# Optimization experiments

Measured on AMD Instinct MI355X. Metric: run time of the kernel, lower is better.

## Reference

```python
import jax, jax.numpy as jnp
import numpy as np

VOCAB, EMB, HID, T, B = 10000, 1500, 1500, 35, 64
FORGET_BIAS = 1.0

def setup_inputs() -> dict:
    key = jax.random.key(0)
    ks = jax.random.split(key, 8)
    s = 0.02
    return {
        'x': jax.random.randint(ks[0], (T, B), 0, VOCAB),
        'y': jax.random.randint(ks[1], (T, B), 0, VOCAB),
        'embedding': jax.random.normal(ks[2], (VOCAB, EMB), jnp.float32) * s,
        'W0': jax.random.normal(ks[3], (EMB + HID, 4 * HID), jnp.float32) * s,
        'b0': jnp.zeros((4 * HID,), jnp.float32),
        'W1': jax.random.normal(ks[4], (2 * HID, 4 * HID), jnp.float32) * s,
        'b1': jnp.zeros((4 * HID,), jnp.float32),
        'softmax_w': jax.random.normal(ks[5], (HID, VOCAB), jnp.float32) * 0.1,
        'softmax_b': jnp.zeros((VOCAB,), jnp.float32),
    }

def _lstm_step(c, h, x, W, b):
    # TF LSTMCell: z = [x, h] @ W + b; gate order i, j, f, o; forget_bias added to f
    z = jnp.concatenate([x, h], axis=-1) @ W + b
    i, j, f, o = jnp.split(z, 4, axis=-1)
    c_new = c * jax.nn.sigmoid(f + FORGET_BIAS) + jax.nn.sigmoid(i) * jnp.tanh(j)
    h_new = jnp.tanh(c_new) * jax.nn.sigmoid(o)
    return c_new, h_new

def reference(x, y, embedding, W0, b0, W1, b1, softmax_w, softmax_b):
    inputs = embedding[x]  # [T, B, EMB] (time_major)
    zeros = jnp.zeros((B, HID), inputs.dtype)
    init = (zeros, zeros, zeros, zeros)  # (c0, h0, c1, h1)

    def step(carry, xt):
        c0, h0, c1, h1 = carry
        c0, h0 = _lstm_step(c0, h0, xt, W0, b0)
        c1, h1 = _lstm_step(c1, h1, h0, W1, b1)
        return (c0, h0, c1, h1), h1

    _, outputs = jax.lax.scan(step, init, inputs)  # [T, B, HID]
    logits = outputs.reshape(-1, HID) @ softmax_w + softmax_b  # [T*B, VOCAB]
    logp = jax.nn.log_softmax(logits, axis=-1)
    tgt = y.reshape(-1)
    nll = -jnp.take_along_axis(logp, tgt[:, None], axis=-1)[:, 0]
    loss = jnp.sum(nll) / B  # sequence_loss_by_example with unit weights, / batch_size
    return loss
```

## Files before the change

kernel.cpp:

```cpp
#include <hip/hip_runtime.h>
#include <math.h>

#define TT 35
#define BB 64
#define EMB 1500
#define HID 1500
#define VOCAB 10000
#define KT 3072
#define KG 768
#define NCH 24
#define KH 1536
#define KGH 384
#define NCHH 12
#define KLP 1504
#define NBLK 158
#define MROWS 2240
#define MPAD 2304
#define LBLK 94
#define ZXN 6000
#define FORGET_BIAS 1.0f

typedef __bf16 bf16x8 __attribute__((ext_vector_type(8)));
typedef float f32x4 __attribute__((ext_vector_type(4)));

__device__ __forceinline__ unsigned short f2bf(float f) {
    unsigned int u = __builtin_bit_cast(unsigned int, f);
    u += 0x7fffu + ((u >> 16) & 1u);
    return (unsigned short)(u >> 16);
}
__device__ __forceinline__ float bf2f(unsigned short u) {
    unsigned int v = ((unsigned int)u) << 16;
    return __builtin_bit_cast(float, v);
}
__device__ __forceinline__ float sigmoidf_(float x) { return 1.0f / (1.0f + expf(-x)); }

#define GLOAD_LDS16(gp, lp) __builtin_amdgcn_global_load_lds( \
    (const __attribute__((address_space(1))) void*)(gp),      \
    (__attribute__((address_space(3))) void*)(lp), 16, 0, 0)

__global__ __launch_bounds__(256) void convT(const float* __restrict__ W,
                                             unsigned short* __restrict__ WT,
                                             int K, int N, int KP) {
    __shared__ float tile[32][33];
    int tx = threadIdx.x, ty = threadIdx.y;
    int n0 = blockIdx.x * 32, k0 = blockIdx.y * 32;
#pragma unroll
    for (int i = 0; i < 4; ++i) {
        int k = k0 + ty + 8 * i, n = n0 + tx;
        tile[ty + 8 * i][tx] = (k < K && n < N) ? W[(size_t)k * N + n] : 0.f;
    }
    __syncthreads();
#pragma unroll
    for (int i = 0; i < 4; ++i) {
        int n = n0 + ty + 8 * i, k = k0 + tx;
        if (n < N) WT[(size_t)n * KP + k] = f2bf(tile[tx][ty + 8 * i]);
    }
}

__global__ __launch_bounds__(256) void embed_kernel(const int* __restrict__ x,
                                                    const float* __restrict__ emb,
                                                    unsigned short* __restrict__ Ae) {
    int tok = blockIdx.x;
    int v = x[tok];
    const float* src = emb + (size_t)v * EMB;
    unsigned short* dst = Ae + (size_t)tok * KH;
    for (int i = threadIdx.x; i < EMB; i += 256) dst[i] = f2bf(src[i]);
}

__global__ __launch_bounds__(256) void zx_gemm(const unsigned short* __restrict__ A,
                                               const unsigned short* __restrict__ WT,
                                               unsigned short* __restrict__ Zx) {
    __shared__ __align__(16) unsigned char smem[32768];
    int orig = blockIdx.x;
    int xcd = orig & 7, j = orig >> 3;
    int mb, bn;
    if (xcd < 7) { bn = xcd * 6 + j % 6; mb = j / 6; }
    else { if (j >= 90) return; bn = 42 + j % 5; mb = j / 5; }
    int n0 = bn * 128;

    int tid = threadIdx.x;
    int wv = tid >> 6, lane = tid & 63;
    int wr = wv >> 1, wc = wv & 1;
    int quad = lane >> 4, l16 = lane & 15;
    int rr = lane >> 2;
    int ks = (lane & 3) ^ (rr & 3);
    const unsigned short* gA[2]; const unsigned short* gB[2];
    int ldsA[2], ldsB[2];
#pragma unroll
    for (int i = 0; i < 2; ++i) {
        int r16 = wv * 2 + i;
        int ra = mb * 128 + r16 * 16 + rr;
        gA[i] = A + (size_t)ra * KH + ks * 8;
        ldsA[i] = r16 * 1024;
        int rb = n0 + r16 * 16 + rr;
        if (rb > 5999) rb = 5999;
        gB[i] = WT + (size_t)rb * KH + ks * 8;
        ldsB[i] = 8192 + r16 * 1024;
    }
    int sw16 = (quad ^ (l16 & 3)) * 16;
    int aoff[4], boff[4];
#pragma unroll
    for (int f = 0; f < 4; ++f) {
        aoff[f] = (wr * 64 + f * 16 + l16) * 64 + sw16;
        boff[f] = 8192 + (wc * 64 + f * 16 + l16) * 64 + sw16;
    }
    f32x4 acc[4][4];
#pragma unroll
    for (int i = 0; i < 4; ++i)
#pragma unroll
        for (int jj = 0; jj < 4; ++jj) acc[i][jj] = (f32x4){0.f, 0.f, 0.f, 0.f};

#pragma unroll
    for (int i = 0; i < 2; ++i) {
        GLOAD_LDS16(gA[i], smem + ldsA[i]);
        GLOAD_LDS16(gB[i], smem + ldsB[i]);
    }
    __syncthreads();
    for (int c = 0; c < KH / 32; ++c) {
        int buf = c & 1;
        if (c + 1 < KH / 32) {
            int ob = (buf ^ 1) * 16384;
#pragma unroll
            for (int i = 0; i < 2; ++i) {
                GLOAD_LDS16(gA[i] + (c + 1) * 32, smem + ob + ldsA[i]);
                GLOAD_LDS16(gB[i] + (c + 1) * 32, smem + ob + ldsB[i]);
            }
        }
        const unsigned char* base = smem + buf * 16384;
        bf16x8 a[4], b[4];
#pragma unroll
        for (int f = 0; f < 4; ++f) {
            a[f] = *(const bf16x8*)(base + aoff[f]);
            b[f] = *(const bf16x8*)(base + boff[f]);
        }
#pragma unroll
        for (int ar = 0; ar < 4; ++ar)
#pragma unroll
            for (int cb = 0; cb < 4; ++cb)
                acc[ar][cb] = __builtin_amdgcn_mfma_f32_16x16x32_bf16(a[ar], b[cb], acc[ar][cb], 0, 0, 0);
        __syncthreads();
    }
#pragma unroll
    for (int ar = 0; ar < 4; ++ar)
#pragma unroll
        for (int cb = 0; cb < 4; ++cb)
#pragma unroll
            for (int r2 = 0; r2 < 4; ++r2) {
                int row = mb * 128 + wr * 64 + ar * 16 + quad * 4 + r2;
                int col = n0 + wc * 64 + cb * 16 + l16;
                if (col < ZXN) Zx[(size_t)row * ZXN + col] = f2bf(acc[ar][cb][r2]);
            }
}

__global__ __launch_bounds__(1024) void lstm_pair(
        const unsigned short* __restrict__ A_0, const unsigned short* __restrict__ WT_0,
        const float* __restrict__ bias_0, float* __restrict__ cst_0,
        unsigned short* __restrict__ d1_0, int s1_0, unsigned short* __restrict__ d2_0, int s2_0,
        const unsigned short* __restrict__ zx_0,
        const unsigned short* __restrict__ A_1, const unsigned short* __restrict__ WT_1,
        const float* __restrict__ bias_1, float* __restrict__ cst_1,
        unsigned short* __restrict__ d1_1, int s1_1, unsigned short* __restrict__ d2_1, int s2_1) {
    __shared__ __align__(16) unsigned char smem[131072];

    const unsigned short* A;  const unsigned short* WT;
    const float* bias;        float* cst;
    unsigned short* d1; int s1; unsigned short* d2; int s2;
    const unsigned short* zx;
    int nb, kstr, kgK, nch;
    if (blockIdx.x < LBLK) {
        if (!A_0) return;
        A = A_0; WT = WT_0; bias = bias_0; cst = cst_0;
        d1 = d1_0; s1 = s1_0; d2 = d2_0; s2 = s2_0;
        zx = zx_0; kstr = KH; kgK = KGH; nch = NCHH;
        nb = blockIdx.x;
    } else {
        if (!A_1) return;
        A = A_1; WT = WT_1; bias = bias_1; cst = cst_1;
        d1 = d1_1; s1 = s1_1; d2 = d2_1; s2 = s2_1;
        zx = nullptr; kstr = KT; kgK = KG; nch = NCH;
        nb = blockIdx.x - LBLK;
    }

    int tid = threadIdx.x;
    int wv = tid >> 6, lane = tid & 63;
    int mt = wv & 3, kg = wv >> 2;
    int quad = lane >> 4, l16 = lane & 15;
    int col = nb * 16 + l16;

    int rr = lane >> 2, p = lane & 3;
    int sp = p ^ (rr & 3);
    int kbase = kg * kgK;
    int q0 = mt * 2, q1 = q0 + 1;
    const unsigned short* gp[2];
    int ldsoff[2];
#pragma unroll
    for (int ii = 0; ii < 2; ++ii) {
        int q = ii ? q1 : q0;
        if (q < 4) {
            gp[ii] = A + (size_t)(16 * q + rr) * kstr + kbase + sp * 8;
        } else {
            int g = q - 4;
            int ci = nb * 16 + rr; if (ci > HID - 1) ci = HID - 1;
            gp[ii] = WT + (size_t)(g * HID + ci) * kstr + kbase + sp * 8;
        }
        ldsoff[ii] = ((q >> 2) * 4 + kg) * 4096 + (q & 3) * 1024;
    }

    int swz = (quad ^ (l16 & 3)) * 16;
    int aoff = (0 * 4 + kg) * 4096 + (mt * 16 + l16) * 64 + swz;
    int boff = (1 * 4 + kg) * 4096 + l16 * 64 + swz;

    f32x4 acc0 = {0.f,0.f,0.f,0.f}, acc1 = acc0, acc2 = acc0, acc3 = acc0;

#pragma unroll
    for (int ci = 0; ci < 3; ++ci) {
        GLOAD_LDS16(gp[0] + ci * 32, smem + ci * 32768 + ldsoff[0]);
        GLOAD_LDS16(gp[1] + ci * 32, smem + ci * 32768 + ldsoff[1]);
    }

    for (int c = 0; c < nch; ++c) {
        asm volatile("s_waitcnt vmcnt(4)" ::: "memory");
        __builtin_amdgcn_sched_barrier(0);
        __builtin_amdgcn_s_barrier();
        int cs = (c + 3 < nch) ? (c + 3) : (nch - 1);
        int bs_ = (c + 3) & 3;
        GLOAD_LDS16(gp[0] + cs * 32, smem + bs_ * 32768 + ldsoff[0]);
        GLOAD_LDS16(gp[1] + cs * 32, smem + bs_ * 32768 + ldsoff[1]);
        const unsigned char* base = smem + (c & 3) * 32768;
        bf16x8 a  = *(const bf16x8*)(base + aoff);
        bf16x8 b0 = *(const bf16x8*)(base + boff);
        bf16x8 b1 = *(const bf16x8*)(base + boff + 1024);
        bf16x8 b2 = *(const bf16x8*)(base + boff + 2048);
        bf16x8 b3 = *(const bf16x8*)(base + boff + 3072);
        __builtin_amdgcn_s_setprio(1);
        acc0 = __builtin_amdgcn_mfma_f32_16x16x32_bf16(a, b0, acc0, 0, 0, 0);
        acc1 = __builtin_amdgcn_mfma_f32_16x16x32_bf16(a, b1, acc1, 0, 0, 0);
        acc2 = __builtin_amdgcn_mfma_f32_16x16x32_bf16(a, b2, acc2, 0, 0, 0);
        acc3 = __builtin_amdgcn_mfma_f32_16x16x32_bf16(a, b3, acc3, 0, 0, 0);
        __builtin_amdgcn_s_setprio(0);
    }
    asm volatile("s_waitcnt vmcnt(0)" ::: "memory");
    __builtin_amdgcn_sched_barrier(0);
    __syncthreads();

    float* red = (float*)smem;
    if (kg > 0) {
        int w = (kg - 1) * 4 + mt;
#pragma unroll
        for (int r = 0; r < 4; ++r) {
            red[(w * 64 + lane) * 16 + r]      = acc0[r];
            red[(w * 64 + lane) * 16 + 4 + r]  = acc1[r];
            red[(w * 64 + lane) * 16 + 8 + r]  = acc2[r];
            red[(w * 64 + lane) * 16 + 12 + r] = acc3[r];
        }
    }
    __syncthreads();
    if (kg == 0) {
#pragma unroll
        for (int k2 = 0; k2 < 3; ++k2) {
            int w = k2 * 4 + mt;
#pragma unroll
            for (int r = 0; r < 4; ++r) {
                acc0[r] += red[(w * 64 + lane) * 16 + r];
                acc1[r] += red[(w * 64 + lane) * 16 + 4 + r];
                acc2[r] += red[(w * 64 + lane) * 16 + 8 + r];
                acc3[r] += red[(w * 64 + lane) * 16 + 12 + r];
            }
        }
        if (col < HID) {
            float bi = bias[col], bj = bias[HID + col];
            float bf_ = bias[2 * HID + col], bo = bias[3 * HID + col];
#pragma unroll
            for (int r = 0; r < 4; ++r) {
                int row = mt * 16 + quad * 4 + r;
                float zi = acc0[r] + bi;
                float zj = acc1[r] + bj;
                float zf = acc2[r] + bf_;
                float zo = acc3[r] + bo;
                if (zx) {
                    const unsigned short* zr = zx + (size_t)row * ZXN;
                    zi += bf2f(zr[col]);
                    zj += bf2f(zr[HID + col]);
                    zf += bf2f(zr[2 * HID + col]);
                    zo += bf2f(zr[3 * HID + col]);
                }
                int ci = row * HID + col;
                float cn = cst[ci] * sigmoidf_(zf + FORGET_BIAS) + sigmoidf_(zi) * tanhf(zj);
                float hn = tanhf(cn) * sigmoidf_(zo);
                cst[ci] = cn;
                unsigned short hb = f2bf(hn);
                d1[(size_t)row * s1 + col] = hb;
                if (d2) d2[(size_t)row * s2 + col] = hb;
            }
        }
    }
}

__global__ __launch_bounds__(256) void logits_fold(const unsigned short* __restrict__ A,
                                                   const unsigned short* __restrict__ WT,
                                                   const float* __restrict__ sb,
                                                   const int* __restrict__ y,
                                                   float2* __restrict__ partials,
                                                   float* __restrict__ tgtlog) {
    __shared__ __align__(16) unsigned char smem[32768];

    int orig = blockIdx.x;
    int xcd = orig & 7, j = orig >> 3;
    int mb, bn;
    if (xcd < 7) { bn = xcd * 10 + j % 10; mb = j / 10; }
    else { if (j >= 162) return; bn = 70 + j % 9; mb = j / 9; }
    int n0 = bn * 128;

    int tid = threadIdx.x;
    int wv = tid >> 6, lane = tid & 63;
    int wr = wv >> 1, wc = wv & 1;
    int quad = lane >> 4, l16 = lane & 15;

    int rr = lane >> 2;
    int ks = (lane & 3) ^ (rr & 3);
    const unsigned short* gA[2]; const unsigned short* gB[2];
    int ldsA[2], ldsB[2];
#pragma unroll
    for (int i = 0; i < 2; ++i) {
        int r16 = wv * 2 + i;
        int ra = mb * 128 + r16 * 16 + rr;
        gA[i] = A + (size_t)ra * KLP + ks * 8;
        ldsA[i] = r16 * 1024;
        int rb = n0 + r16 * 16 + rr;
        if (rb > VOCAB - 1) rb = VOCAB - 1;
        gB[i] = WT + (size_t)rb * KLP + ks * 8;
        ldsB[i] = 8192 + r16 * 1024;
    }

    int sw16 = (quad ^ (l16 & 3)) * 16;
    int aoff[4], boff[4];
#pragma unroll
    for (int f = 0; f < 4; ++f) {
        aoff[f] = (wr * 64 + f * 16 + l16) * 64 + sw16;
        boff[f] = 8192 + (wc * 64 + f * 16 + l16) * 64 + sw16;
    }

    f32x4 acc[4][4];
#pragma unroll
    for (int i = 0; i < 4; ++i)
#pragma unroll
        for (int jj = 0; jj < 4; ++jj) acc[i][jj] = (f32x4){0.f, 0.f, 0.f, 0.f};

#pragma unroll
    for (int i = 0; i < 2; ++i) {
        GLOAD_LDS16(gA[i], smem + ldsA[i]);
        GLOAD_LDS16(gB[i], smem + ldsB[i]);
    }
    __syncthreads();

    for (int c = 0; c < KLP / 32; ++c) {
        int buf = c & 1;
        if (c + 1 < KLP / 32) {
            int ob = (buf ^ 1) * 16384;
#pragma unroll
            for (int i = 0; i < 2; ++i) {
                GLOAD_LDS16(gA[i] + (c + 1) * 32, smem + ob + ldsA[i]);
                GLOAD_LDS16(gB[i] + (c + 1) * 32, smem + ob + ldsB[i]);
            }
        }
        const unsigned char* base = smem + buf * 16384;
        bf16x8 a[4], b[4];
#pragma unroll
        for (int f = 0; f < 4; ++f) {
            a[f] = *(const bf16x8*)(base + aoff[f]);
            b[f] = *(const bf16x8*)(base + boff[f]);
        }
#pragma unroll
        for (int ar = 0; ar < 4; ++ar)
#pragma unroll
            for (int cb = 0; cb < 4; ++cb)
                acc[ar][cb] = __builtin_amdgcn_mfma_f32_16x16x32_bf16(a[ar], b[cb], acc[ar][cb], 0, 0, 0);
        __syncthreads();
    }

    int colv[4]; float bs[4];
#pragma unroll
    for (int cb = 0; cb < 4; ++cb) {
        int c = n0 + wc * 64 + cb * 16 + l16;
        colv[cb] = c;
        int cc = (c < VOCAB) ? c : (VOCAB - 1);
        bs[cb] = sb[cc];
    }
    int nb2 = bn * 2 + wc;
#pragma unroll
    for (int ar = 0; ar < 4; ++ar) {
#pragma unroll
        for (int r2 = 0; r2 < 4; ++r2) {
            float v0 = acc[ar][0][r2] + bs[0];
            float v1 = acc[ar][1][r2] + bs[1];
            float v2 = acc[ar][2][r2] + bs[2];
            float v3 = acc[ar][3][r2] + bs[3];
            if (colv[0] >= VOCAB) v0 = -1e30f;
            if (colv[1] >= VOCAB) v1 = -1e30f;
            if (colv[2] >= VOCAB) v2 = -1e30f;
            if (colv[3] >= VOCAB) v3 = -1e30f;
            int row = mb * 128 + wr * 64 + ar * 16 + quad * 4 + r2;
            int t = y[row < MROWS ? row : 0];
            float tv = -1e30f;
            if (colv[0] == t) tv = v0;
            if (colv[1] == t) tv = v1;
            if (colv[2] == t) tv = v2;
            if (colv[3] == t) tv = v3;
            float mx = fmaxf(fmaxf(v0, v1), fmaxf(v2, v3));
#pragma unroll
            for (int d = 1; d < 16; d <<= 1) mx = fmaxf(mx, __shfl_xor(mx, d, 64));
            float sum = expf(v0 - mx) + expf(v1 - mx) + expf(v2 - mx) + expf(v3 - mx);
#pragma unroll
            for (int d = 1; d < 16; d <<= 1) sum += __shfl_xor(sum, d, 64);
#pragma unroll
            for (int d = 1; d < 16; d <<= 1) tv = fmaxf(tv, __shfl_xor(tv, d, 64));
            if (l16 == 0 && row < MROWS) {
                partials[(size_t)row * NBLK + nb2] = make_float2(mx, sum);
                if (tv > -5e29f) tgtlog[row] = tv;
            }
        }
    }
}

__global__ __launch_bounds__(64) void nll_reduce(const float2* __restrict__ partials,
                                                 const float* __restrict__ tgtlog,
                                                 float* __restrict__ nll) {
    int row = blockIdx.x;
    int lane = threadIdx.x;
    float2 loc[3];
    int cnt = 0;
    float m = -1e30f;
    for (int i = lane; i < NBLK; i += 64) {
        float2 p = partials[(size_t)row * NBLK + i];
        loc[cnt++] = p;
        m = fmaxf(m, p.x);
    }
#pragma unroll
    for (int d = 1; d < 64; d <<= 1) m = fmaxf(m, __shfl_xor(m, d, 64));
    float s = 0.f;
    for (int jj = 0; jj < cnt; ++jj) s += loc[jj].y * expf(loc[jj].x - m);
#pragma unroll
    for (int d = 1; d < 64; d <<= 1) s += __shfl_xor(s, d, 64);
    if (lane == 0) nll[row] = -(tgtlog[row] - m - logf(s));
}

__global__ __launch_bounds__(256) void loss_kernel(const float* __restrict__ nll,
                                                   float* __restrict__ out) {
    __shared__ float red[256];
    int tid = threadIdx.x;
    float s = 0.f;
    for (int i = tid; i < TT * BB; i += 256) s += nll[i];
    red[tid] = s; __syncthreads();
    for (int st = 128; st > 0; st >>= 1) { if (tid < st) red[tid] += red[tid + st]; __syncthreads(); }
    if (tid == 0) out[0] = red[0] / (float)BB;
}

extern "C" void kernel_launch(void* const* d_in, const int* in_sizes, int n_in,
                              void* d_out, int out_size, void* d_ws, size_t ws_size,
                              hipStream_t stream) {
    const int*   x   = (const int*)d_in[0];
    const int*   y   = (const int*)d_in[1];
    const float* emb = (const float*)d_in[2];
    const float* W0  = (const float*)d_in[3];
    const float* b0  = (const float*)d_in[4];
    const float* W1  = (const float*)d_in[5];
    const float* b1  = (const float*)d_in[6];
    const float* sw  = (const float*)d_in[7];
    const float* sb  = (const float*)d_in[8];
    float* out = (float*)d_out;

    char* p = (char*)d_ws;
    unsigned short* Ae   = (unsigned short*)p; p += (size_t)MPAD * KH * 2;
    unsigned short* A1   = (unsigned short*)p; p += (size_t)2 * BB * KT * 2;
    unsigned short* H0   = (unsigned short*)p; p += (size_t)2 * BB * KH * 2;
    unsigned short* outs = (unsigned short*)p; p += (size_t)MPAD * KLP * 2;
    float* c0 = (float*)p; p += (size_t)BB * HID * 4;
    float* c1 = (float*)p; p += (size_t)BB * HID * 4;
    size_t zero_bytes = (size_t)(p - (char*)d_ws);
    unsigned short* Zx   = (unsigned short*)p; p += (size_t)MPAD * ZXN * 2;
    unsigned short* WxT0 = (unsigned short*)p; p += (size_t)6000 * KH * 2;
    unsigned short* WhT0 = (unsigned short*)p; p += (size_t)6000 * KH * 2;
    unsigned short* WbT1 = (unsigned short*)p; p += (size_t)6000 * KT * 2;
    unsigned short* swT  = (unsigned short*)p; p += (size_t)VOCAB * KLP * 2;
    float2* partials = (float2*)p; p += (size_t)TT * BB * NBLK * 8;
    float* tgtlog = (float*)p; p += (size_t)TT * BB * 4;
    float* nll    = (float*)p;

    hipMemsetAsync(d_ws, 0, zero_bytes, stream);

    dim3 cblk(32, 8);
    convT<<<dim3(188, 48), cblk, 0, stream>>>(W0, WxT0, 1500, 6000, KH);
    convT<<<dim3(188, 48), cblk, 0, stream>>>(W0 + (size_t)1500 * 6000, WhT0, 1500, 6000, KH);
    convT<<<dim3(188, 96), cblk, 0, stream>>>(W1, WbT1, 3000, 6000, KT);
    convT<<<dim3(313, 47), cblk, 0, stream>>>(sw, swT, HID, VOCAB, KLP);

    embed_kernel<<<TT * BB, 256, 0, stream>>>(x, emb, Ae);
    zx_gemm<<<864, 256, 0, stream>>>(Ae, WxT0, Zx);

    for (int k = 0; k <= TT; ++k) {
        const unsigned short* A0t = (k < TT) ? H0 + (size_t)((k - 1) & 1) * BB * KH : nullptr;
        unsigned short* d1_0 = A1 + (size_t)(k & 1) * BB * KT;
        unsigned short* d2_0 = H0 + (size_t)(k & 1) * BB * KH;
        const unsigned short* zx0 = Zx + (size_t)k * BB * ZXN;

        const unsigned short* A1t = (k >= 1) ? A1 + (size_t)((k - 1) & 1) * BB * KT : nullptr;
        unsigned short* d1_1 = A1 + (size_t)(k & 1) * BB * KT + HID;
        unsigned short* d2_1 = (k >= 1) ? outs + (size_t)(k - 1) * BB * KLP : nullptr;

        lstm_pair<<<188, 1024, 0, stream>>>(A0t, WhT0, b0, c0, d1_0, KT, d2_0, KH, zx0,
                                            A1t, WbT1, b1, c1, d1_1, KT, d2_1, KLP);
    }

    logits_fold<<<1440, 256, 0, stream>>>(outs, swT, sb, y, partials, tgtlog);
    nll_reduce<<<TT * BB, 64, 0, stream>>>(partials, tgtlog, nll);
    loss_kernel<<<1, 256, 0, stream>>>(nll, out);
}
```

Before: 1.303 ms.

## Rebalance LSTM step split-K across blocks and deepen GEMM pipelines

Layer-1 work in each step is now split along K: the 94 layer-0 blocks also compute the tail slice of layer 1's K range. The other 94 blocks take the larger head slice. The two halves are combined through a global partial buffer and an atomic arrival counter, and the last block to arrive does the gate math. This is meant to even out per-block work, which was lopsided because layer-0 blocks had half the K of layer-1 blocks. The zx and logits GEMMs move from a 2-stage to a 4-stage global-to-LDS pipeline with setprio around the MFMAs, and the LDS swizzle gains an extra XOR term to reduce bank conflicts. The cost is extra global traffic, fences and atomics on every step.

```diff
diff --git a/kernel.cpp b/kernel.cpp
--- a/kernel.cpp
+++ b/kernel.cpp
@@ -7,11 +7,7 @@
 #define HID 1500
 #define VOCAB 10000
 #define KT 3072
-#define KG 768
-#define NCH 24
 #define KH 1536
-#define KGH 384
-#define NCHH 12
 #define KLP 1504
 #define NBLK 158
 #define MROWS 2240
@@ -19,6 +15,13 @@
 #define LBLK 94
 #define ZXN 6000
 #define FORGET_BIAS 1.0f
+#define NCH0 12
+#define KG0 384
+#define NCH1M 18
+#define KG1M 576
+#define NCH1T 6
+#define KG1T 192
+#define KW1T 2304
 
 typedef __bf16 bf16x8 __attribute__((ext_vector_type(8)));
 typedef float f32x4 __attribute__((ext_vector_type(4)));
@@ -67,129 +70,15 @@
     for (int i = threadIdx.x; i < EMB; i += 256) dst[i] = f2bf(src[i]);
 }
 
-__global__ __launch_bounds__(256) void zx_gemm(const unsigned short* __restrict__ A,
-                                               const unsigned short* __restrict__ WT,
-                                               unsigned short* __restrict__ Zx) {
-    __shared__ __align__(16) unsigned char smem[32768];
-    int orig = blockIdx.x;
-    int xcd = orig & 7, j = orig >> 3;
-    int mb, bn;
-    if (xcd < 7) { bn = xcd * 6 + j % 6; mb = j / 6; }
-    else { if (j >= 90) return; bn = 42 + j % 5; mb = j / 5; }
-    int n0 = bn * 128;
-
-    int tid = threadIdx.x;
-    int wv = tid >> 6, lane = tid & 63;
-    int wr = wv >> 1, wc = wv & 1;
-    int quad = lane >> 4, l16 = lane & 15;
+__device__ __forceinline__ void run_job(const unsigned short* __restrict__ A, int As,
+                                        const unsigned short* __restrict__ W, int Ws,
+                                        int kwin, int kgK, int nch, int nb,
+                                        unsigned char* smem,
+                                        int mt, int kg, int lane, int l16,
+                                        int sp, int swz,
+                                        f32x4& acc0, f32x4& acc1, f32x4& acc2, f32x4& acc3) {
     int rr = lane >> 2;
-    int ks = (lane & 3) ^ (rr & 3);
-    const unsigned short* gA[2]; const unsigned short* gB[2];
-    int ldsA[2], ldsB[2];
-#pragma unroll
-    for (int i = 0; i < 2; ++i) {
-        int r16 = wv * 2 + i;
-        int ra = mb * 128 + r16 * 16 + rr;
-        gA[i] = A + (size_t)ra * KH + ks * 8;
-        ldsA[i] = r16 * 1024;
-        int rb = n0 + r16 * 16 + rr;
-        if (rb > 5999) rb = 5999;
-        gB[i] = WT + (size_t)rb * KH + ks * 8;
-        ldsB[i] = 8192 + r16 * 1024;
-    }
-    int sw16 = (quad ^ (l16 & 3)) * 16;
-    int aoff[4], boff[4];
-#pragma unroll
-    for (int f = 0; f < 4; ++f) {
-        aoff[f] = (wr * 64 + f * 16 + l16) * 64 + sw16;
-        boff[f] = 8192 + (wc * 64 + f * 16 + l16) * 64 + sw16;
-    }
-    f32x4 acc[4][4];
-#pragma unroll
-    for (int i = 0; i < 4; ++i)
-#pragma unroll
-        for (int jj = 0; jj < 4; ++jj) acc[i][jj] = (f32x4){0.f, 0.f, 0.f, 0.f};
-
-#pragma unroll
-    for (int i = 0; i < 2; ++i) {
-        GLOAD_LDS16(gA[i], smem + ldsA[i]);
-        GLOAD_LDS16(gB[i], smem + ldsB[i]);
-    }
-    __syncthreads();
-    for (int c = 0; c < KH / 32; ++c) {
-        int buf = c & 1;
-        if (c + 1 < KH / 32) {
-            int ob = (buf ^ 1) * 16384;
-#pragma unroll
-            for (int i = 0; i < 2; ++i) {
-                GLOAD_LDS16(gA[i] + (c + 1) * 32, smem + ob + ldsA[i]);
-                GLOAD_LDS16(gB[i] + (c + 1) * 32, smem + ob + ldsB[i]);
-            }
-        }
-        const unsigned char* base = smem + buf * 16384;
-        bf16x8 a[4], b[4];
-#pragma unroll
-        for (int f = 0; f < 4; ++f) {
-            a[f] = *(const bf16x8*)(base + aoff[f]);
-            b[f] = *(const bf16x8*)(base + boff[f]);
-        }
-#pragma unroll
-        for (int ar = 0; ar < 4; ++ar)
-#pragma unroll
-            for (int cb = 0; cb < 4; ++cb)
-                acc[ar][cb] = __builtin_amdgcn_mfma_f32_16x16x32_bf16(a[ar], b[cb], acc[ar][cb], 0, 0, 0);
-        __syncthreads();
-    }
-#pragma unroll
-    for (int ar = 0; ar < 4; ++ar)
-#pragma unroll
-        for (int cb = 0; cb < 4; ++cb)
-#pragma unroll
-            for (int r2 = 0; r2 < 4; ++r2) {
-                int row = mb * 128 + wr * 64 + ar * 16 + quad * 4 + r2;
-                int col = n0 + wc * 64 + cb * 16 + l16;
-                if (col < ZXN) Zx[(size_t)row * ZXN + col] = f2bf(acc[ar][cb][r2]);
-            }
-}
-
-__global__ __launch_bounds__(1024) void lstm_pair(
-        const unsigned short* __restrict__ A_0, const unsigned short* __restrict__ WT_0,
-        const float* __restrict__ bias_0, float* __restrict__ cst_0,
-        unsigned short* __restrict__ d1_0, int s1_0, unsigned short* __restrict__ d2_0, int s2_0,
-        const unsigned short* __restrict__ zx_0,
-        const unsigned short* __restrict__ A_1, const unsigned short* __restrict__ WT_1,
-        const float* __restrict__ bias_1, float* __restrict__ cst_1,
-        unsigned short* __restrict__ d1_1, int s1_1, unsigned short* __restrict__ d2_1, int s2_1) {
-    __shared__ __align__(16) unsigned char smem[131072];
-
-    const unsigned short* A;  const unsigned short* WT;
-    const float* bias;        float* cst;
-    unsigned short* d1; int s1; unsigned short* d2; int s2;
-    const unsigned short* zx;
-    int nb, kstr, kgK, nch;
-    if (blockIdx.x < LBLK) {
-        if (!A_0) return;
-        A = A_0; WT = WT_0; bias = bias_0; cst = cst_0;
-        d1 = d1_0; s1 = s1_0; d2 = d2_0; s2 = s2_0;
-        zx = zx_0; kstr = KH; kgK = KGH; nch = NCHH;
-        nb = blockIdx.x;
-    } else {
-        if (!A_1) return;
-        A = A_1; WT = WT_1; bias = bias_1; cst = cst_1;
-        d1 = d1_1; s1 = s1_1; d2 = d2_1; s2 = s2_1;
-        zx = nullptr; kstr = KT; kgK = KG; nch = NCH;
-        nb = blockIdx.x - LBLK;
-    }
-
-    int tid = threadIdx.x;
-    int wv = tid >> 6, lane = tid & 63;
-    int mt = wv & 3, kg = wv >> 2;
-    int quad = lane >> 4, l16 = lane & 15;
-    int col = nb * 16 + l16;
-
-    int rr = lane >> 2, p = lane & 3;
-    int sp = p ^ (rr & 3);
-    int kbase = kg * kgK;
+    int kbase = kwin + kg * kgK;
     int q0 = mt * 2, q1 = q0 + 1;
     const unsigned short* gp[2];
     int ldsoff[2];
@@ -197,27 +86,23 @@
     for (int ii = 0; ii < 2; ++ii) {
         int q = ii ? q1 : q0;
         if (q < 4) {
-            gp[ii] = A + (size_t)(16 * q + rr) * kstr + kbase + sp * 8;
+            gp[ii] = A + (size_t)(16 * q + rr) * As + kbase + sp * 8;
         } else {
-            int g = q - 4;
             int ci = nb * 16 + rr; if (ci > HID - 1) ci = HID - 1;
-            gp[ii] = WT + (size_t)(g * HID + ci) * kstr + kbase + sp * 8;
+            gp[ii] = W + (size_t)((q - 4) * HID + ci) * Ws + kbase + sp * 8;
         }
         ldsoff[ii] = ((q >> 2) * 4 + kg) * 4096 + (q & 3) * 1024;
     }
-
-    int swz = (quad ^ (l16 & 3)) * 16;
-    int aoff = (0 * 4 + kg) * 4096 + (mt * 16 + l16) * 64 + swz;
-    int boff = (1 * 4 + kg) * 4096 + l16 * 64 + swz;
-
-    f32x4 acc0 = {0.f,0.f,0.f,0.f}, acc1 = acc0, acc2 = acc0, acc3 = acc0;
+    int aoff = kg * 4096 + (mt * 16 + l16) * 64 + swz;
+    int boff = (4 + kg) * 4096 + l16 * 64 + swz;
+
+    acc0 = (f32x4){0.f, 0.f, 0.f, 0.f}; acc1 = acc0; acc2 = acc0; acc3 = acc0;
 
 #pragma unroll
     for (int ci = 0; ci < 3; ++ci) {
         GLOAD_LDS16(gp[0] + ci * 32, smem + ci * 32768 + ldsoff[0]);
         GLOAD_LDS16(gp[1] + ci * 32, smem + ci * 32768 + ldsoff[1]);
     }
-
     for (int c = 0; c < nch; ++c) {
         asm volatile("s_waitcnt vmcnt(4)" ::: "memory");
         __builtin_amdgcn_sched_barrier(0);
@@ -242,7 +127,10 @@
     asm volatile("s_waitcnt vmcnt(0)" ::: "memory");
     __builtin_amdgcn_sched_barrier(0);
     __syncthreads();
-
+}
+
+__device__ __forceinline__ void kg_reduce(unsigned char* smem, int kg, int mt, int lane,
+                                          f32x4& acc0, f32x4& acc1, f32x4& acc2, f32x4& acc3) {
     float* red = (float*)smem;
     if (kg > 0) {
         int w = (kg - 1) * 4 + mt;
@@ -267,33 +155,218 @@
                 acc3[r] += red[(w * 64 + lane) * 16 + 12 + r];
             }
         }
-        if (col < HID) {
-            float bi = bias[col], bj = bias[HID + col];
-            float bf_ = bias[2 * HID + col], bo = bias[3 * HID + col];
+    }
+    __syncthreads();
+}
+
+__global__ __launch_bounds__(1024) void lstm_pair(
+        const unsigned short* __restrict__ A_0, const unsigned short* __restrict__ WT_0,
+        const float* __restrict__ bias_0, float* __restrict__ cst_0,
+        unsigned short* __restrict__ d1_0, int s1_0, unsigned short* __restrict__ d2_0, int s2_0,
+        const unsigned short* __restrict__ zx_0,
+        const unsigned short* __restrict__ A_1, const unsigned short* __restrict__ WT_1,
+        const float* __restrict__ bias_1, float* __restrict__ cst_1,
+        unsigned short* __restrict__ d1_1, int s1_1, unsigned short* __restrict__ d2_1, int s2_1,
+        float* __restrict__ zpart, int* __restrict__ zflag) {
+    __shared__ __align__(16) unsigned char smem[131072];
+    __shared__ int oldflag;
+
+    int tid = threadIdx.x;
+    int wv = tid >> 6, lane = tid & 63;
+    int mt = wv & 3, kg = wv >> 2;
+    int quad = lane >> 4, l16 = lane & 15;
+    int rr = lane >> 2, p = lane & 3;
+    int sp = p ^ (rr & 3) ^ ((rr >> 2) & 3);
+    int swz = (quad ^ (l16 & 3) ^ ((l16 >> 2) & 3)) * 16;
+
+    bool isA = (blockIdx.x >= LBLK);
+    int cb = isA ? (int)blockIdx.x - LBLK : (int)blockIdx.x;
+    bool doL1 = (A_1 != nullptr);
+    f32x4 acc0, acc1, acc2, acc3;
+
+    if (isA) {
+        if (A_0) {
+            run_job(A_0, KH, WT_0, KH, 0, KG0, NCH0, cb, smem,
+                    mt, kg, lane, l16, sp, swz, acc0, acc1, acc2, acc3);
+            kg_reduce(smem, kg, mt, lane, acc0, acc1, acc2, acc3);
+            if (kg == 0) {
+                int col = cb * 16 + l16;
+                if (col < HID) {
+                    float bi = bias_0[col], bj = bias_0[HID + col];
+                    float bf_ = bias_0[2 * HID + col], bo = bias_0[3 * HID + col];
+#pragma unroll
+                    for (int r = 0; r < 4; ++r) {
+                        int row = mt * 16 + quad * 4 + r;
+                        const unsigned short* zr = zx_0 + (size_t)row * ZXN;
+                        float zi = acc0[r] + bi + bf2f(zr[col]);
+                        float zj = acc1[r] + bj + bf2f(zr[HID + col]);
+                        float zf = acc2[r] + bf_ + bf2f(zr[2 * HID + col]);
+                        float zo = acc3[r] + bo + bf2f(zr[3 * HID + col]);
+                        int ci = row * HID + col;
+                        float cn = cst_0[ci] * sigmoidf_(zf + FORGET_BIAS) + sigmoidf_(zi) * tanhf(zj);
+                        float hn = tanhf(cn) * sigmoidf_(zo);
+                        cst_0[ci] = cn;
+                        unsigned short hb = f2bf(hn);
+                        d1_0[(size_t)row * s1_0 + col] = hb;
+                        d2_0[(size_t)row * s2_0 + col] = hb;
+                    }
+                }
+            }
+        }
+        if (!doL1) return;
+        run_job(A_1, KT, WT_1, KT, KW1T, KG1T, NCH1T, cb, smem,
+                mt, kg, lane, l16, sp, swz, acc0, acc1, acc2, acc3);
+        kg_reduce(smem, kg, mt, lane, acc0, acc1, acc2, acc3);
+    } else {
+        if (!doL1) return;
+        run_job(A_1, KT, WT_1, KT, 0, KG1M, NCH1M, cb, smem,
+                mt, kg, lane, l16, sp, swz, acc0, acc1, acc2, acc3);
+        kg_reduce(smem, kg, mt, lane, acc0, acc1, acc2, acc3);
+    }
+
+    int half = isA ? 1 : 0;
+    float* zp = zpart + ((size_t)cb * 2 + half) * 4096;
+    if (kg == 0) {
+#pragma unroll
+        for (int r = 0; r < 4; ++r) {
+            zp[(mt * 64 + lane) * 16 + r]      = acc0[r];
+            zp[(mt * 64 + lane) * 16 + 4 + r]  = acc1[r];
+            zp[(mt * 64 + lane) * 16 + 8 + r]  = acc2[r];
+            zp[(mt * 64 + lane) * 16 + 12 + r] = acc3[r];
+        }
+    }
+    __threadfence();
+    __syncthreads();
+    if (tid == 0) oldflag = atomicAdd(&zflag[cb], 1);
+    __syncthreads();
+    if (oldflag == 1) {
+        __threadfence();
+        if (kg == 0) {
+            const float* zq = zpart + ((size_t)cb * 2 + (half ^ 1)) * 4096;
 #pragma unroll
             for (int r = 0; r < 4; ++r) {
-                int row = mt * 16 + quad * 4 + r;
-                float zi = acc0[r] + bi;
-                float zj = acc1[r] + bj;
-                float zf = acc2[r] + bf_;
-                float zo = acc3[r] + bo;
-                if (zx) {
-                    const unsigned short* zr = zx + (size_t)row * ZXN;
-                    zi += bf2f(zr[col]);
-                    zj += bf2f(zr[HID + col]);
-                    zf += bf2f(zr[2 * HID + col]);
-                    zo += bf2f(zr[3 * HID + col]);
+                acc0[r] += zq[(mt * 64 + lane) * 16 + r];
+                acc1[r] += zq[(mt * 64 + lane) * 16 + 4 + r];
+                acc2[r] += zq[(mt * 64 + lane) * 16 + 8 + r];
+                acc3[r] += zq[(mt * 64 + lane) * 16 + 12 + r];
+            }
+            int col = cb * 16 + l16;
+            if (col < HID) {
+                float bi = bias_1[col], bj = bias_1[HID + col];
+                float bf_ = bias_1[2 * HID + col], bo = bias_1[3 * HID + col];
+#pragma unroll
+                for (int r = 0; r < 4; ++r) {
+                    int row = mt * 16 + quad * 4 + r;
+                    float zi = acc0[r] + bi;
+                    float zj = acc1[r] + bj;
+                    float zf = acc2[r] + bf_;
+                    float zo = acc3[r] + bo;
+                    int ci = row * HID + col;
+                    float cn = cst_1[ci] * sigmoidf_(zf + FORGET_BIAS) + sigmoidf_(zi) * tanhf(zj);
+                    float hn = tanhf(cn) * sigmoidf_(zo);
+                    cst_1[ci] = cn;
+                    unsigned short hb = f2bf(hn);
+                    d1_1[(size_t)row * s1_1 + col] = hb;
+                    if (d2_1) d2_1[(size_t)row * s2_1 + col] = hb;
                 }
-                int ci = row * HID + col;
-                float cn = cst[ci] * sigmoidf_(zf + FORGET_BIAS) + sigmoidf_(zi) * tanhf(zj);
-                float hn = tanhf(cn) * sigmoidf_(zo);
-                cst[ci] = cn;
-                unsigned short hb = f2bf(hn);
-                d1[(size_t)row * s1 + col] = hb;
-                if (d2) d2[(size_t)row * s2 + col] = hb;
             }
         }
-    }
+        __syncthreads();
+        if (tid == 0) zflag[cb] = 0;
+    }
+}
+
+__global__ __launch_bounds__(256) void zx_gemm(const unsigned short* __restrict__ A,
+                                               const unsigned short* __restrict__ WT,
+                                               unsigned short* __restrict__ Zx) {
+    __shared__ __align__(16) unsigned char smem[65536];
+    int orig = blockIdx.x;
+    int xcd = orig & 7, j = orig >> 3;
+    int mb, bn;
+    if (xcd < 7) { bn = xcd * 6 + j % 6; mb = j / 6; }
+    else { if (j >= 90) return; bn = 42 + j % 5; mb = j / 5; }
+    int n0 = bn * 128;
+
+    int tid = threadIdx.x;
+    int wv = tid >> 6, lane = tid & 63;
+    int wr = wv >> 1, wc = wv & 1;
+    int quad = lane >> 4, l16 = lane & 15;
+    int rr = lane >> 2;
+    int ks = (lane & 3) ^ (rr & 3) ^ ((rr >> 2) & 3);
+    const unsigned short* gA[2]; const unsigned short* gB[2];
+    int ldsA[2], ldsB[2];
+#pragma unroll
+    for (int i = 0; i < 2; ++i) {
+        int r16 = wv * 2 + i;
+        int ra = mb * 128 + r16 * 16 + rr;
+        gA[i] = A + (size_t)ra * KH + ks * 8;
+        ldsA[i] = r16 * 1024;
+        int rb = n0 + r16 * 16 + rr;
+        if (rb > 5999) rb = 5999;
+        gB[i] = WT + (size_t)rb * KH + ks * 8;
+        ldsB[i] = 8192 + r16 * 1024;
+    }
+    int sw16 = (quad ^ (l16 & 3) ^ ((l16 >> 2) & 3)) * 16;
+    int aoff[4], boff[4];
+#pragma unroll
+    for (int f = 0; f < 4; ++f) {
+        aoff[f] = (wr * 64 + f * 16 + l16) * 64 + sw16;
+        boff[f] = 8192 + (wc * 64 + f * 16 + l16) * 64 + sw16;
+    }
+    f32x4 acc[4][4];
+#pragma unroll
+    for (int i = 0; i < 4; ++i)
+#pragma unroll
+        for (int jj = 0; jj < 4; ++jj) acc[i][jj] = (f32x4){0.f, 0.f, 0.f, 0.f};
+
+    const int NCHZ = KH / 32;
+#pragma unroll
+    for (int ci = 0; ci < 3; ++ci)
+#pragma unroll
+        for (int i = 0; i < 2; ++i) {
+            GLOAD_LDS16(gA[i] + ci * 32, smem + ci * 16384 + ldsA[i]);
+            GLOAD_LDS16(gB[i] + ci * 32, smem + ci * 16384 + ldsB[i]);
+        }
+    for (int c = 0; c < NCHZ; ++c) {
+        asm volatile("s_waitcnt vmcnt(8)" ::: "memory");
+        __builtin_amdgcn_sched_barrier(0);
+        __builtin_amdgcn_s_barrier();
+        int cs = (c + 3 < NCHZ) ? (c + 3) : (NCHZ - 1);
+        int ob = ((c + 3) & 3) * 16384;
+#pragma unroll
+        for (int i = 0; i < 2; ++i) {
+            GLOAD_LDS16(gA[i] + cs * 32, smem + ob + ldsA[i]);
+            GLOAD_LDS16(gB[i] + cs * 32, smem + ob + ldsB[i]);
+        }
+        const unsigned char* base = smem + (c & 3) * 16384;
+        bf16x8 a[4], b[4];
+#pragma unroll
+        for (int f = 0; f < 4; ++f) {
+            a[f] = *(const bf16x8*)(base + aoff[f]);
+            b[f] = *(const bf16x8*)(base + boff[f]);
+        }
+        __builtin_amdgcn_s_setprio(1);
+#pragma unroll
+        for (int ar = 0; ar < 4; ++ar)
+#pragma unroll
+            for (int cbv = 0; cbv < 4; ++cbv)
+                acc[ar][cbv] = __builtin_amdgcn_mfma_f32_16x16x32_bf16(a[ar], b[cbv], acc[ar][cbv], 0, 0, 0);
+        __builtin_amdgcn_s_setprio(0);
+    }
+    asm volatile("s_waitcnt vmcnt(0)" ::: "memory");
+    __builtin_amdgcn_sched_barrier(0);
+    __syncthreads();
+
+#pragma unroll
+    for (int ar = 0; ar < 4; ++ar)
+#pragma unroll
+        for (int cbv = 0; cbv < 4; ++cbv)
+#pragma unroll
+            for (int r2 = 0; r2 < 4; ++r2) {
+                int row = mb * 128 + wr * 64 + ar * 16 + quad * 4 + r2;
+                int col = n0 + wc * 64 + cbv * 16 + l16;
+                if (col < ZXN) Zx[(size_t)row * ZXN + col] = f2bf(acc[ar][cbv][r2]);
+            }
 }
 
 __global__ __launch_bounds__(256) void logits_fold(const unsigned short* __restrict__ A,
@@ -302,7 +375,7 @@
                                                    const int* __restrict__ y,
                                                    float2* __restrict__ partials,
                                                    float* __restrict__ tgtlog) {
-    __shared__ __align__(16) unsigned char smem[32768];
+    __shared__ __align__(16) unsigned char smem[65536];
 
     int orig = blockIdx.x;
     int xcd = orig & 7, j = orig >> 3;
@@ -317,7 +390,7 @@
     int quad = lane >> 4, l16 = lane & 15;
 
     int rr = lane >> 2;
-    int ks = (lane & 3) ^ (rr & 3);
+    int ks = (lane & 3) ^ (rr & 3) ^ ((rr >> 2) & 3);
     const unsigned short* gA[2]; const unsigned short* gB[2];
     int ldsA[2], ldsB[2];
 #pragma unroll
@@ -332,7 +405,7 @@
         ldsB[i] = 8192 + r16 * 1024;
     }
 
-    int sw16 = (quad ^ (l16 & 3)) * 16;
+    int sw16 = (quad ^ (l16 & 3) ^ ((l16 >> 2) & 3)) * 16;
     int aoff[4], boff[4];
 #pragma unroll
     for (int f = 0; f < 4; ++f) {
@@ -346,45 +419,51 @@
 #pragma unroll
         for (int jj = 0; jj < 4; ++jj) acc[i][jj] = (f32x4){0.f, 0.f, 0.f, 0.f};
 
-#pragma unroll
-    for (int i = 0; i < 2; ++i) {
-        GLOAD_LDS16(gA[i], smem + ldsA[i]);
-        GLOAD_LDS16(gB[i], smem + ldsB[i]);
-    }
-    __syncthreads();
-
-    for (int c = 0; c < KLP / 32; ++c) {
-        int buf = c & 1;
-        if (c + 1 < KLP / 32) {
-            int ob = (buf ^ 1) * 16384;
-#pragma unroll
-            for (int i = 0; i < 2; ++i) {
-                GLOAD_LDS16(gA[i] + (c + 1) * 32, smem + ob + ldsA[i]);
-                GLOAD_LDS16(gB[i] + (c + 1) * 32, smem + ob + ldsB[i]);
-            }
-        }
-        const unsigned char* base = smem + buf * 16384;
+    const int NCHL = KLP / 32;
+#pragma unroll
+    for (int ci = 0; ci < 3; ++ci)
+#pragma unroll
+        for (int i = 0; i < 2; ++i) {
+            GLOAD_LDS16(gA[i] + ci * 32, smem + ci * 16384 + ldsA[i]);
+            GLOAD_LDS16(gB[i] + ci * 32, smem + ci * 16384 + ldsB[i]);
+        }
+    for (int c = 0; c < NCHL; ++c) {
+        asm volatile("s_waitcnt vmcnt(8)" ::: "memory");
+        __builtin_amdgcn_sched_barrier(0);
+        __builtin_amdgcn_s_barrier();
+        int cs = (c + 3 < NCHL) ? (c + 3) : (NCHL - 1);
+        int ob = ((c + 3) & 3) * 16384;
+#pragma unroll
+        for (int i = 0; i < 2; ++i) {
+            GLOAD_LDS16(gA[i] + cs * 32, smem + ob + ldsA[i]);
+            GLOAD_LDS16(gB[i] + cs * 32, smem + ob + ldsB[i]);
+        }
+        const unsigned char* base = smem + (c & 3) * 16384;
         bf16x8 a[4], b[4];
 #pragma unroll
         for (int f = 0; f < 4; ++f) {
             a[f] = *(const bf16x8*)(base + aoff[f]);
             b[f] = *(const bf16x8*)(base + boff[f]);
         }
+        __builtin_amdgcn_s_setprio(1);
 #pragma unroll
         for (int ar = 0; ar < 4; ++ar)
 #pragma unroll
-            for (int cb = 0; cb < 4; ++cb)
-                acc[ar][cb] = __builtin_amdgcn_mfma_f32_16x16x32_bf16(a[ar], b[cb], acc[ar][cb], 0, 0, 0);
-        __syncthreads();
-    }
+            for (int cbv = 0; cbv < 4; ++cbv)
+                acc[ar][cbv] = __builtin_amdgcn_mfma_f32_16x16x32_bf16(a[ar], b[cbv], acc[ar][cbv], 0, 0, 0);
+        __builtin_amdgcn_s_setprio(0);
+    }
+    asm volatile("s_waitcnt vmcnt(0)" ::: "memory");
+    __builtin_amdgcn_sched_barrier(0);
+    __syncthreads();
 
     int colv[4]; float bs[4];
 #pragma unroll
-    for (int cb = 0; cb < 4; ++cb) {
-        int c = n0 + wc * 64 + cb * 16 + l16;
-        colv[cb] = c;
+    for (int cbv = 0; cbv < 4; ++cbv) {
+        int c = n0 + wc * 64 + cbv * 16 + l16;
+        colv[cbv] = c;
         int cc = (c < VOCAB) ? c : (VOCAB - 1);
-        bs[cb] = sb[cc];
+        bs[cbv] = sb[cc];
     }
     int nb2 = bn * 2 + wc;
 #pragma unroll
@@ -476,6 +555,8 @@
     unsigned short* outs = (unsigned short*)p; p += (size_t)MPAD * KLP * 2;
     float* c0 = (float*)p; p += (size_t)BB * HID * 4;
     float* c1 = (float*)p; p += (size_t)BB * HID * 4;
+    float* zpart = (float*)p; p += (size_t)94 * 2 * 4096 * 4;
+    int*   zflag = (int*)p;  p += 256 * 4;
     size_t zero_bytes = (size_t)(p - (char*)d_ws);
     unsigned short* Zx   = (unsigned short*)p; p += (size_t)MPAD * ZXN * 2;
     unsigned short* WxT0 = (unsigned short*)p; p += (size_t)6000 * KH * 2;
@@ -508,7 +589,8 @@
         unsigned short* d2_1 = (k >= 1) ? outs + (size_t)(k - 1) * BB * KLP : nullptr;
 
         lstm_pair<<<188, 1024, 0, stream>>>(A0t, WhT0, b0, c0, d1_0, KT, d2_0, KH, zx0,
-                                            A1t, WbT1, b1, c1, d1_1, KT, d2_1, KLP);
+                                            A1t, WbT1, b1, c1, d1_1, KT, d2_1, KLP,
+                                            zpart, zflag);
     }
 
     logits_fold<<<1440, 256, 0, stream>>>(outs, swT, sb, y, partials, tgtlog);
```

Result: slower. 4.584 ms (+251.7%).
